# Kernel tuning notes

Measured on AMD Instinct MI355X. Metric: run time of the kernel, lower is better.

## Reference

```python
import jax, jax.numpy as jnp
import numpy as np

A = 1.0  # hard-sigmoid slope 'a'


def hard_sigm(x):
    return jnp.clip((A * x + 1.0) * 0.5, 0.0, 1.0)


def _cell(c, h_bottom, h, h_top, z, zb, U11, U21, W01, b, H):
    # batch-major equivalent of torch.mm(U, h) with h:(H,B) -> h@(U.T):(B,4H+1)
    s = (1.0 - z) * (h @ U11.T) + zb * (h_bottom @ W01.T) + b
    if U21 is not None:
        s = s + z * (h_top @ U21.T)
    f = jax.nn.sigmoid(s[:, 0:H])
    i = jax.nn.sigmoid(s[:, H:2 * H])
    o = jax.nn.sigmoid(s[:, 2 * H:3 * H])
    g = jnp.tanh(s[:, 3 * H:4 * H])
    z_hat = hard_sigm(s[:, 4 * H:4 * H + 1])  # (B,1)
    c_new = z * (i * g) + (1.0 - z) * (1.0 - zb) * c + (1.0 - z) * zb * (f * c + i * g)
    tc = jnp.tanh(c_new)
    h_new = z * o * tc + (1.0 - z) * (1.0 - zb) * h + (1.0 - z) * zb * o * tc
    return h_new, c_new, z_hat


def setup_inputs() -> dict:
    key = jax.random.key(0)
    ks = jax.random.split(key, 8)
    B, T, D = 256, 512, 128
    H1, H2 = 512, 512
    stdv = 1.0 / np.sqrt(H1)
    u = lambda k, shp: jax.random.uniform(k, shp, jnp.float32, -stdv, stdv)
    return {
        'inputs': jax.random.normal(ks[0], (B, T, D), jnp.float32),
        'U11_1': u(ks[1], (4 * H1 + 1, H1)),
        'U21_1': u(ks[2], (4 * H1 + 1, H2)),
        'W01_1': u(ks[3], (4 * H1 + 1, D)),
        'b1': u(ks[4], (4 * H1 + 1,)),
        'U11_2': u(ks[5], (4 * H2 + 1, H2)),
        'W01_2': u(ks[6], (4 * H2 + 1, H1)),
        'b2': u(ks[7], (4 * H2 + 1,)),
    }


def reference(inputs, U11_1, U21_1, W01_1, b1, U11_2, W01_2, b2):
    B, T, D = inputs.shape
    H1 = (b1.shape[0] - 1) // 4
    H2 = (b2.shape[0] - 1) // 4
    dt = inputs.dtype
    h1 = jnp.zeros((B, H1), dt); c1 = jnp.zeros((B, H1), dt); z1 = jnp.zeros((B, 1), dt)
    h2 = jnp.zeros((B, H2), dt); c2 = jnp.zeros((B, H2), dt); z2 = jnp.zeros((B, 1), dt)
    z_one = jnp.ones((B, 1), dt)

    def step(carry, x_t):
        h1, c1, z1, h2, c2, z2 = carry
        h1, c1, z1 = _cell(c1, x_t, h1, h2, z1, z_one, U11_1, U21_1, W01_1, b1, H1)
        h2, c2, z2 = _cell(c2, h1, h2, None, z2, z1, U11_2, None, W01_2, b2, H2)
        return (h1, c1, z1, h2, c2, z2), h2 * z2

    xs = jnp.swapaxes(inputs, 0, 1)  # (T,B,D)
    _, ys = jax.lax.scan(step, (h1, c1, z1, h2, c2, z2), xs)
    # dropout is identity in eval mode
    return jnp.swapaxes(ys, 0, 1)  # (B,T,H2)
```

## Files before the change

### kernel.cpp

```cpp
#include <hip/hip_runtime.h>

#define TT 512
#define BB 256
#define DD 128
#define HH 512
#define KA 1152
#define KB 1024
#define NKA 36
#define NKB 32

#define OFF_WPA  0ull
#define SZ_WPA   (128ull*NKA*2ull*512ull*2ull)
#define OFF_WPB  (OFF_WPA + SZ_WPA)
#define SZ_WPB   (128ull*NKB*2ull*512ull*2ull)
#define OFF_WZFA (OFF_WPB + SZ_WPB)
#define SZ_WZFA  (36ull*512ull*2ull)
#define OFF_WZFB (OFF_WZFA + SZ_WZFA)
#define SZ_WZFB  (32ull*512ull*2ull)
#define OFF_BP1  (OFF_WZFB + SZ_WZFB)
#define OFF_BP2  (OFF_BP1 + 8192ull)
#define OFF_BZ   (OFF_BP2 + 8192ull)
#define OFF_CNT  (OFF_BZ + 256ull)
#define OFF_A1   (OFF_CNT + 4096ull)
#define OFF_A2   (OFF_A1 + 2ull*524288ull)
#define OFF_B1   (OFF_A2 + 524288ull)
#define OFF_B2   (OFF_B1 + 2ull*524288ull)
#define OFF_END  (OFF_B2 + 524288ull)

#define PLSTR 131072

typedef __bf16 bf16x8 __attribute__((ext_vector_type(8)));
typedef float  f32x4  __attribute__((ext_vector_type(4)));
typedef unsigned short u16;

__device__ __forceinline__ u16 bf_bits(__bf16 h) {
  union { __bf16 b; u16 u; } cv; cv.b = h; return cv.u;
}
__device__ __forceinline__ float sigmoidf_(float v) { return 1.f / (1.f + __expf(-v)); }

__device__ __forceinline__ void st_uc(u16* p, u16 v) {
  unsigned vv = v;
  asm volatile("global_store_short %0, %1, off sc0 sc1" :: "v"(p), "v"(vv) : "memory");
}
__device__ __forceinline__ void split_st_uc(u16* hi, u16* lo, float v) {
  __bf16 h = (__bf16)v;
  __bf16 l = (__bf16)(v - (float)h);
  st_uc(hi, bf_bits(h));
  st_uc(lo, bf_bits(l));
}
__device__ __forceinline__ void drain_vmem() {
  asm volatile("s_waitcnt vmcnt(0)" ::: "memory");
}

__device__ __forceinline__ void gload_lds16_uc(const void* g, void* l) {
  __builtin_amdgcn_global_load_lds((const __attribute__((address_space(1))) unsigned int*)g,
                                   (__attribute__((address_space(3))) unsigned int*)l, 16, 0, 19);
}

__global__ void pack_w(const float* __restrict__ U11_1, const float* __restrict__ U21_1,
                       const float* __restrict__ W01_1, const float* __restrict__ U11_2,
                       const float* __restrict__ W01_2, u16* __restrict__ wp) {
  unsigned i = blockIdx.x * 256u + threadIdx.x;
  const unsigned NWA = 128u * NKA * 2u * 512u;
  const unsigned NWB = 128u * NKB * 2u * 512u;
  if (i >= NWA + NWB) return;
  float w; unsigned s;
  if (i < NWA) {
    unsigned lane = (i >> 3) & 63u, e = i & 7u; s = (i >> 9) & 1u;
    unsigned blk = i >> 10, kb = blk % NKA, colblk = blk / NKA;
    unsigned c = colblk * 16u + (lane & 15u);
    unsigned n = (c & 3u) * 512u + (c >> 2);
    unsigned k = kb * 32u + (lane >> 4) * 8u + e;
    w = (k < 512u)  ? U11_1[n * 512u + k]
      : (k < 1024u) ? U21_1[n * 512u + (k - 512u)]
                    : W01_1[n * 128u + (k - 1024u)];
  } else {
    unsigned j = i - NWA;
    unsigned lane = (j >> 3) & 63u, e = j & 7u; s = (j >> 9) & 1u;
    unsigned blk = j >> 10, kb = blk % NKB, colblk = blk / NKB;
    unsigned c = colblk * 16u + (lane & 15u);
    unsigned n = (c & 3u) * 512u + (c >> 2);
    unsigned k = kb * 32u + (lane >> 4) * 8u + e;
    w = (k < 512u) ? U11_2[n * 512u + k] : W01_2[n * 512u + (k - 512u)];
  }
  __bf16 hi = (__bf16)w;
  __bf16 v = s ? (__bf16)(w - (float)hi) : hi;
  wp[i] = bf_bits(v);
}

__global__ void pack_wz(const float* __restrict__ U11_1, const float* __restrict__ U21_1,
                        const float* __restrict__ W01_1, const float* __restrict__ U11_2,
                        const float* __restrict__ W01_2,
                        u16* __restrict__ wzfa, u16* __restrict__ wzfb) {
  unsigned i = blockIdx.x * 256u + threadIdx.x;
  const unsigned NZA = 36u * 512u, NZB = 32u * 512u;
  if (i >= NZA + NZB) return;
  const bool isA = i < NZA;
  unsigned j = isA ? i : i - NZA;
  unsigned e = j & 7u, lane = (j >> 3) & 63u, kb = j >> 9;
  unsigned col = lane & 15u;
  unsigned k = kb * 32u + (lane >> 4) * 8u + e;
  float wz;
  if (isA) {
    wz = (k < 512u)  ? U11_1[2048u*512u + k]
       : (k < 1024u) ? U21_1[2048u*512u + (k-512u)]
                     : W01_1[2048u*128u + (k-1024u)];
  } else {
    wz = (k < 512u) ? U11_2[2048u*512u + k] : W01_2[2048u*512u + (k-512u)];
  }
  u16 out = 0;
  if (col == 0u) out = bf_bits((__bf16)wz);
  else if (col == 1u) { __bf16 h = (__bf16)wz; out = bf_bits((__bf16)(wz - (float)h)); }
  (isA ? wzfa : wzfb)[j] = out;
}

__global__ void pack_bias(const float* __restrict__ b1, const float* __restrict__ b2,
                          float* __restrict__ bp1, float* __restrict__ bp2,
                          float* __restrict__ bz) {
  unsigned i = blockIdx.x * 256u + threadIdx.x;
  if (i < 2048u) bp1[i] = b1[(i & 3u)*512u + (i >> 2)];
  else if (i < 4096u) { unsigned c = i - 2048u; bp2[c] = b2[(c & 3u)*512u + (c >> 2)]; }
  else if (i == 4096u) bz[0] = b1[2048];
  else if (i == 4097u) bz[1] = b2[2048];
}

__global__ void init_zero(char* __restrict__ wsb) {
  size_t i = (size_t)blockIdx.x * 256u + threadIdx.x;
  size_t n = (OFF_END - OFF_CNT) / 4u;
  if (i < n) ((unsigned*)(wsb + OFF_CNT))[i] = 0u;
}

__global__ __launch_bounds__(512, 2) void hmlstm_kernel(const float* __restrict__ x,
                                                        char* __restrict__ wsb,
                                                        float* __restrict__ y) {
  const int tid  = threadIdx.x;
  const int lane = tid & 63;
  const int nw   = __builtin_amdgcn_readfirstlane(tid >> 6);
  const int bid  = blockIdx.x;
  const int ntg  = (bid & 7) * 2 + (bid >> 7);
  const int mg   = (bid >> 3) & 15;
  const int b0   = mg * 16;

  const u16* wpA  = (const u16*)(wsb + OFF_WPA);
  const u16* wpB  = (const u16*)(wsb + OFF_WPB);
  const u16* wzfA = (const u16*)(wsb + OFF_WZFA);
  const u16* wzfB = (const u16*)(wsb + OFF_WZFB);
  const float* bp1 = (const float*)(wsb + OFF_BP1);
  const float* bp2 = (const float*)(wsb + OFF_BP2);
  const float bz1 = ((const float*)(wsb + OFF_BZ))[0];
  const float bz2 = ((const float*)(wsb + OFF_BZ))[1];
  unsigned* cnt = (unsigned*)(wsb + OFF_CNT) + mg * 64;
  u16* A1b[2] = { (u16*)(wsb + OFF_A1), (u16*)(wsb + OFF_A1 + 524288ull) };
  u16* A2b    =   (u16*)(wsb + OFF_A2);
  u16* B1b[2] = { (u16*)(wsb + OFF_B1), (u16*)(wsb + OFF_B1 + 524288ull) };
  u16* B2b    =   (u16*)(wsb + OFF_B2);

  __shared__ u16 stgA[2][2][16][64][8];
  __shared__ u16 stgB[2][2][16][64][8];
  __shared__ float ls_s[16][132];
  __shared__ float zp[3][16];

  const int kgp   = lane >> 4;
  const int row16 = lane & 15;
  const int er = tid >> 5, eu = tid & 31;
  const int erow = b0 + er;
  const int ku = ntg * 32 + eu;
  const size_t pidx = ((size_t)(ku >> 3) * 256 + erow) * 8 + (ku & 7);

  const u16* wbA = wpA + (size_t)(ntg*8 + nw) * (NKA*1024u) + lane*8;
  const u16* wbB = wpB + (size_t)(ntg*8 + nw) * (NKB*1024u) + lane*8;
  const u16* wzA = wzfA + lane*8;
  const u16* wzB = wzfB + lane*8;

  float c1r = 0.f, c2r = 0.f, h2r = 0.f;
  float z1p = 0.f, z2p = 0.f, z1c = 0.f;
  unsigned bar_tgt = 16u;
  int p = 0;

  for (int t = 0; t < TT; ++t) {
    if (t == 0) {
      for (int j = 0; j < 4; ++j) {
        int i = nw*4 + j; int spl = i >> 4, kq = i & 15;
        const u16* src = A1b[0] + spl*PLSTR + ((size_t)((kq*4 + kgp)*256 + b0 + row16))*8;
        gload_lds16_uc(src, &stgA[0][spl][kq][0][0]);
      }
    }
    for (int j = 0; j < 4; ++j) {
      int i = nw*4 + j; int spl = i >> 4, kq = i & 15;
      const u16* src = A2b + spl*PLSTR + ((size_t)((kq*4 + kgp)*256 + b0 + row16))*8;
      gload_lds16_uc(src, &stgA[1][spl][kq][0][0]);
    }
    for (int j = 0; j < 4; ++j) {
      int i = nw*4 + j; int spl = i >> 4, kq = i & 15;
      const u16* src = B1b[p] + spl*PLSTR + ((size_t)((kq*4 + kgp)*256 + b0 + row16))*8;
      gload_lds16_uc(src, &stgB[0][spl][kq][0][0]);
    }
    bf16x8 xah[4], xal[4];
    {
      const float* xp = x + ((size_t)(b0 + row16) * TT + t) * DD + kgp*8;
      for (int k4 = 0; k4 < 4; ++k4) {
        float4 v0 = *(const float4*)(xp + k4*32);
        float4 v1 = *(const float4*)(xp + k4*32 + 4);
        float vv[8] = {v0.x,v0.y,v0.z,v0.w,v1.x,v1.y,v1.z,v1.w};
        for (int e = 0; e < 8; ++e) {
          __bf16 h = (__bf16)vv[e];
          xah[k4][e] = h;
          xal[k4][e] = (__bf16)(vv[e] - (float)h);
        }
      }
    }
    __syncthreads();

    {
      f32x4 acc0={0,0,0,0}, acc1={0,0,0,0}, acc2={0,0,0,0};
      f32x4 az={0,0,0,0};
      #pragma unroll 4
      for (int kb = 0; kb < 32; ++kb) {
        const u16* sa = &stgA[kb>>4][0][kb&15][lane][0];
        bf16x8 ah = *(const bf16x8*)sa;
        bf16x8 al = *(const bf16x8*)(sa + 8192);
        bf16x8 wh = *(const bf16x8*)(wbA + kb*1024);
        bf16x8 wl = *(const bf16x8*)(wbA + kb*1024 + 512);
        acc0 = __builtin_amdgcn_mfma_f32_16x16x32_bf16(ah, wh, acc0, 0, 0, 0);
        acc1 = __builtin_amdgcn_mfma_f32_16x16x32_bf16(ah, wl, acc1, 0, 0, 0);
        acc2 = __builtin_amdgcn_mfma_f32_16x16x32_bf16(al, wh, acc2, 0, 0, 0);
        if (nw == 0) { bf16x8 zf = *(const bf16x8*)(wzA + kb*512);
                       az = __builtin_amdgcn_mfma_f32_16x16x32_bf16(ah, zf, az, 0, 0, 0); }
        if (nw == 1) { bf16x8 zf = *(const bf16x8*)(wzA + kb*512);
                       az = __builtin_amdgcn_mfma_f32_16x16x32_bf16(al, zf, az, 0, 0, 0); }
      }
      for (int k4 = 0; k4 < 4; ++k4) {
        int kb = 32 + k4;
        bf16x8 ah = xah[k4], al = xal[k4];
        bf16x8 wh = *(const bf16x8*)(wbA + kb*1024);
        bf16x8 wl = *(const bf16x8*)(wbA + kb*1024 + 512);
        acc0 = __builtin_amdgcn_mfma_f32_16x16x32_bf16(ah, wh, acc0, 0, 0, 0);
        acc1 = __builtin_amdgcn_mfma_f32_16x16x32_bf16(ah, wl, acc1, 0, 0, 0);
        acc2 = __builtin_amdgcn_mfma_f32_16x16x32_bf16(al, wh, acc2, 0, 0, 0);
        if (nw == 0) { bf16x8 zf = *(const bf16x8*)(wzA + kb*512);
                       az = __builtin_amdgcn_mfma_f32_16x16x32_bf16(ah, zf, az, 0, 0, 0); }
        if (nw == 1) { bf16x8 zf = *(const bf16x8*)(wzA + kb*512);
                       az = __builtin_amdgcn_mfma_f32_16x16x32_bf16(al, zf, az, 0, 0, 0); }
      }
      f32x4 accs = acc0 + acc1; accs = accs + acc2;
      int cc = nw*16 + (lane & 15);
      int r0 = (lane >> 4) * 4;
      ls_s[r0+0][cc] = accs[0]; ls_s[r0+1][cc] = accs[1];
      ls_s[r0+2][cc] = accs[2]; ls_s[r0+3][cc] = accs[3];
      if (nw == 0 && (lane&15) == 0) {
        for (int j2 = 0; j2 < 4; ++j2) zp[0][r0+j2] = az[j2];
      }
      if (nw == 0 && (lane&15) == 1) {
        for (int j2 = 0; j2 < 4; ++j2) zp[1][r0+j2] = az[j2];
      }
      if (nw == 1 && (lane&15) == 0) {
        for (int j2 = 0; j2 < 4; ++j2) zp[2][r0+j2] = az[j2];
      }
    }
    __syncthreads();
    {
      float zs = zp[0][er] + zp[1][er] + zp[2][er] + bz1;
      float zn = fminf(fmaxf((zs + 1.f)*0.5f, 0.f), 1.f);
      float4 sv = *(const float4*)&ls_s[er][4*eu];
      float4 bb = *(const float4*)&bp1[ntg*128 + 4*eu];
      float f = sigmoidf_(sv.x + bb.x);
      float i = sigmoidf_(sv.y + bb.y);
      float o = sigmoidf_(sv.z + bb.z);
      float g = tanhf(sv.w + bb.w);
      float z = z1p;
      float ig = i * g;
      float cn = z * ig + (1.f - z) * fmaf(f, c1r, ig);
      float hn = o * tanhf(cn);
      c1r = cn;
      z1c = zn; z1p = zn;
      u16* a1w = A1b[p ^ 1];
      split_st_uc(a1w + pidx, a1w + PLSTR + pidx, (1.f - zn) * hn);
      split_st_uc(B2b + pidx, B2b + PLSTR + pidx, zn * hn);
    }
    drain_vmem();
    __syncthreads();
    if (tid == 0) {
      __hip_atomic_fetch_add(cnt, 1u, __ATOMIC_RELAXED, __HIP_MEMORY_SCOPE_AGENT);
      while (__hip_atomic_load(cnt, __ATOMIC_RELAXED, __HIP_MEMORY_SCOPE_AGENT) < bar_tgt)
        __builtin_amdgcn_s_sleep(1);
    }
    bar_tgt += 16u;
    __builtin_amdgcn_s_barrier();

    for (int j = 0; j < 4; ++j) {
      int i = nw*4 + j; int spl = i >> 4, kq = i & 15;
      const u16* src = B2b + spl*PLSTR + ((size_t)((kq*4 + kgp)*256 + b0 + row16))*8;
      gload_lds16_uc(src, &stgB[1][spl][kq][0][0]);
    }
    for (int j = 0; j < 4; ++j) {
      int i = nw*4 + j; int spl = i >> 4, kq = i & 15;
      const u16* src = A1b[p ^ 1] + spl*PLSTR + ((size_t)((kq*4 + kgp)*256 + b0 + row16))*8;
      gload_lds16_uc(src, &stgA[0][spl][kq][0][0]);
    }
    __syncthreads();

    {
      f32x4 acc0={0,0,0,0}, acc1={0,0,0,0}, acc2={0,0,0,0};
      f32x4 az={0,0,0,0};
      #pragma unroll 4
      for (int kb = 0; kb < 32; ++kb) {
        const u16* sa = &stgB[kb>>4][0][kb&15][lane][0];
        bf16x8 ah = *(const bf16x8*)sa;
        bf16x8 al = *(const bf16x8*)(sa + 8192);
        bf16x8 wh = *(const bf16x8*)(wbB + kb*1024);
        bf16x8 wl = *(const bf16x8*)(wbB + kb*1024 + 512);
        acc0 = __builtin_amdgcn_mfma_f32_16x16x32_bf16(ah, wh, acc0, 0, 0, 0);
        acc1 = __builtin_amdgcn_mfma_f32_16x16x32_bf16(ah, wl, acc1, 0, 0, 0);
        acc2 = __builtin_amdgcn_mfma_f32_16x16x32_bf16(al, wh, acc2, 0, 0, 0);
        if (nw == 0) { bf16x8 zf = *(const bf16x8*)(wzB + kb*512);
                       az = __builtin_amdgcn_mfma_f32_16x16x32_bf16(ah, zf, az, 0, 0, 0); }
        if (nw == 1) { bf16x8 zf = *(const bf16x8*)(wzB + kb*512);
                       az = __builtin_amdgcn_mfma_f32_16x16x32_bf16(al, zf, az, 0, 0, 0); }
      }
      f32x4 accs = acc0 + acc1; accs = accs + acc2;
      int cc = nw*16 + (lane & 15);
      int r0 = (lane >> 4) * 4;
      ls_s[r0+0][cc] = accs[0]; ls_s[r0+1][cc] = accs[1];
      ls_s[r0+2][cc] = accs[2]; ls_s[r0+3][cc] = accs[3];
      if (nw == 0 && (lane&15) == 0) {
        for (int j2 = 0; j2 < 4; ++j2) zp[0][r0+j2] = az[j2];
      }
      if (nw == 0 && (lane&15) == 1) {
        for (int j2 = 0; j2 < 4; ++j2) zp[1][r0+j2] = az[j2];
      }
      if (nw == 1 && (lane&15) == 0) {
        for (int j2 = 0; j2 < 4; ++j2) zp[2][r0+j2] = az[j2];
      }
    }
    __syncthreads();
    {
      float zs = zp[0][er] + zp[1][er] + zp[2][er] + bz2;
      float z2n_ = fminf(fmaxf((zs + 1.f)*0.5f, 0.f), 1.f);
      float4 sv = *(const float4*)&ls_s[er][4*eu];
      float4 bb = *(const float4*)&bp2[ntg*128 + 4*eu];
      float f = sigmoidf_(sv.x + bb.x);
      float i = sigmoidf_(sv.y + bb.y);
      float o = sigmoidf_(sv.z + bb.z);
      float g = tanhf(sv.w + bb.w);
      float z = z2p, zb = z1c;
      float ig = i * g;
      float cn = z*ig + (1.f-z)*(1.f-zb)*c2r + (1.f-z)*zb*fmaf(f, c2r, ig);
      float tc = tanhf(cn);
      float ot = o * tc;
      float hn = z*ot + (1.f-z)*(1.f-zb)*h2r + (1.f-z)*zb*ot;
      c2r = cn; h2r = hn;
      z2p = z2n_;
      y[((size_t)erow * TT + t) * HH + ku] = hn * z2n_;
      u16* b1w = B1b[p ^ 1];
      split_st_uc(b1w + pidx, b1w + PLSTR + pidx, (1.f - z2n_) * hn);
      split_st_uc(A2b + pidx, A2b + PLSTR + pidx, z1c * hn);
    }
    drain_vmem();
    __syncthreads();
    if (tid == 0) {
      __hip_atomic_fetch_add(cnt, 1u, __ATOMIC_RELAXED, __HIP_MEMORY_SCOPE_AGENT);
      while (__hip_atomic_load(cnt, __ATOMIC_RELAXED, __HIP_MEMORY_SCOPE_AGENT) < bar_tgt)
        __builtin_amdgcn_s_sleep(1);
    }
    bar_tgt += 16u;
    __builtin_amdgcn_s_barrier();

    p ^= 1;
  }
}

extern "C" void kernel_launch(void* const* d_in, const int* in_sizes, int n_in,
                              void* d_out, int out_size, void* d_ws, size_t ws_size,
                              hipStream_t stream) {
  const float* x     = (const float*)d_in[0];
  const float* U11_1 = (const float*)d_in[1];
  const float* U21_1 = (const float*)d_in[2];
  const float* W01_1 = (const float*)d_in[3];
  const float* b1    = (const float*)d_in[4];
  const float* U11_2 = (const float*)d_in[5];
  const float* W01_2 = (const float*)d_in[6];
  const float* b2    = (const float*)d_in[7];
  char*  wsb = (char*)d_ws;
  float* y   = (float*)d_out;
  (void)in_sizes; (void)n_in; (void)out_size; (void)ws_size;

  u16* wp    = (u16*)(wsb + OFF_WPA);
  u16* wzfa  = (u16*)(wsb + OFF_WZFA);
  u16* wzfb  = (u16*)(wsb + OFF_WZFB);
  float* bp1 = (float*)(wsb + OFF_BP1);
  float* bp2 = (float*)(wsb + OFF_BP2);
  float* bz  = (float*)(wsb + OFF_BZ);

  const unsigned NW = 128u*NKA*2u*512u + 128u*NKB*2u*512u;
  hipLaunchKernelGGL(pack_w, dim3((NW + 255u)/256u), dim3(256), 0, stream,
                     U11_1, U21_1, W01_1, U11_2, W01_2, wp);
  const unsigned NZ = 36u*512u + 32u*512u;
  hipLaunchKernelGGL(pack_wz, dim3((NZ + 255u)/256u), dim3(256), 0, stream,
                     U11_1, U21_1, W01_1, U11_2, W01_2, wzfa, wzfb);
  hipLaunchKernelGGL(pack_bias, dim3(17), dim3(256), 0, stream, b1, b2, bp1, bp2, bz);
  const unsigned n_zero_words = (unsigned)((OFF_END - OFF_CNT) / 4u);
  hipLaunchKernelGGL(init_zero, dim3((n_zero_words + 255u)/256u), dim3(256), 0, stream, wsb);

  const float* xq = x;
  char* wsq = wsb;
  float* yq = y;
  void* kargs[] = { (void*)&xq, (void*)&wsq, (void*)&yq };
  hipLaunchCooperativeKernel((void*)hmlstm_kernel, dim3(256), dim3(512), kargs, 0, stream);
}
```

Before: 15.56 ms.

## Replace atomic-counter grid barrier with per-block flag array and wave-wide polling

The atomic fetch-add counter barrier across the 16 blocks of a batch group is replaced by a flag array: each block writes its phase number to its own slot, and wave 0 polls all 16 slots with uncached loads and a ballot. This removes contention on one atomic and lets a single poll observe every peer. The global-to-LDS load cache-policy bits change from 19 to 17, and the MFMA inner loops unroll 8 instead of 4. The flag protocol depends on uncached stores becoming visible in order after the data stores, and the larger unroll raises register pressure.

```diff
diff --git a/kernel.cpp b/kernel.cpp
--- a/kernel.cpp
+++ b/kernel.cpp
@@ -42,6 +42,15 @@
   unsigned vv = v;
   asm volatile("global_store_short %0, %1, off sc0 sc1" :: "v"(p), "v"(vv) : "memory");
 }
+__device__ __forceinline__ void st_uc_u32(unsigned* p, unsigned v) {
+  asm volatile("global_store_dword %0, %1, off sc0 sc1" :: "v"(p), "v"(v) : "memory");
+}
+__device__ __forceinline__ unsigned ld_uc_u32(const unsigned* p) {
+  unsigned v;
+  asm volatile("global_load_dword %0, %1, off sc0 sc1\n\ts_waitcnt vmcnt(0)"
+               : "=v"(v) : "v"(p) : "memory");
+  return v;
+}
 __device__ __forceinline__ void split_st_uc(u16* hi, u16* lo, float v) {
   __bf16 h = (__bf16)v;
   __bf16 l = (__bf16)(v - (float)h);
@@ -54,7 +63,7 @@
 
 __device__ __forceinline__ void gload_lds16_uc(const void* g, void* l) {
   __builtin_amdgcn_global_load_lds((const __attribute__((address_space(1))) unsigned int*)g,
-                                   (__attribute__((address_space(3))) unsigned int*)l, 16, 0, 19);
+                                   (__attribute__((address_space(3))) unsigned int*)l, 16, 0, 17);
 }
 
 __global__ void pack_w(const float* __restrict__ U11_1, const float* __restrict__ U21_1,
@@ -149,7 +158,7 @@
   const float* bp2 = (const float*)(wsb + OFF_BP2);
   const float bz1 = ((const float*)(wsb + OFF_BZ))[0];
   const float bz2 = ((const float*)(wsb + OFF_BZ))[1];
-  unsigned* cnt = (unsigned*)(wsb + OFF_CNT) + mg * 64;
+  unsigned* flags = (unsigned*)(wsb + OFF_CNT) + mg * 64;
   u16* A1b[2] = { (u16*)(wsb + OFF_A1), (u16*)(wsb + OFF_A1 + 524288ull) };
   u16* A2b    =   (u16*)(wsb + OFF_A2);
   u16* B1b[2] = { (u16*)(wsb + OFF_B1), (u16*)(wsb + OFF_B1 + 524288ull) };
@@ -174,7 +183,6 @@
 
   float c1r = 0.f, c2r = 0.f, h2r = 0.f;
   float z1p = 0.f, z2p = 0.f, z1c = 0.f;
-  unsigned bar_tgt = 16u;
   int p = 0;
 
   for (int t = 0; t < TT; ++t) {
@@ -214,7 +222,7 @@
     {
       f32x4 acc0={0,0,0,0}, acc1={0,0,0,0}, acc2={0,0,0,0};
       f32x4 az={0,0,0,0};
-      #pragma unroll 4
+      #pragma unroll 8
       for (int kb = 0; kb < 32; ++kb) {
         const u16* sa = &stgA[kb>>4][0][kb&15][lane][0];
         bf16x8 ah = *(const bf16x8*)sa;
@@ -279,13 +287,20 @@
     }
     drain_vmem();
     __syncthreads();
-    if (tid == 0) {
-      __hip_atomic_fetch_add(cnt, 1u, __ATOMIC_RELAXED, __HIP_MEMORY_SCOPE_AGENT);
-      while (__hip_atomic_load(cnt, __ATOMIC_RELAXED, __HIP_MEMORY_SCOPE_AGENT) < bar_tgt)
-        __builtin_amdgcn_s_sleep(1);
-    }
-    bar_tgt += 16u;
-    __builtin_amdgcn_s_barrier();
+    {
+      const unsigned tgt = 2u*(unsigned)t + 1u;
+      if (nw == 0) {
+        if (lane == 0) st_uc_u32(&flags[ntg], tgt);
+        const unsigned* fp = flags + (lane & 15);
+        const bool mine = lane < 16;
+        while (true) {
+          unsigned v = mine ? ld_uc_u32(fp) : tgt;
+          if (__ballot(v >= tgt) == ~0ull) break;
+          __builtin_amdgcn_s_sleep(1);
+        }
+      }
+      __builtin_amdgcn_s_barrier();
+    }
 
     for (int j = 0; j < 4; ++j) {
       int i = nw*4 + j; int spl = i >> 4, kq = i & 15;
@@ -302,7 +317,7 @@
     {
       f32x4 acc0={0,0,0,0}, acc1={0,0,0,0}, acc2={0,0,0,0};
       f32x4 az={0,0,0,0};
-      #pragma unroll 4
+      #pragma unroll 8
       for (int kb = 0; kb < 32; ++kb) {
         const u16* sa = &stgB[kb>>4][0][kb&15][lane][0];
         bf16x8 ah = *(const bf16x8*)sa;
@@ -357,13 +372,20 @@
     }
     drain_vmem();
     __syncthreads();
-    if (tid == 0) {
-      __hip_atomic_fetch_add(cnt, 1u, __ATOMIC_RELAXED, __HIP_MEMORY_SCOPE_AGENT);
-      while (__hip_atomic_load(cnt, __ATOMIC_RELAXED, __HIP_MEMORY_SCOPE_AGENT) < bar_tgt)
-        __builtin_amdgcn_s_sleep(1);
-    }
-    bar_tgt += 16u;
-    __builtin_amdgcn_s_barrier();
+    {
+      const unsigned tgt = 2u*(unsigned)t + 2u;
+      if (nw == 0) {
+        if (lane == 0) st_uc_u32(&flags[ntg], tgt);
+        const unsigned* fp = flags + (lane & 15);
+        const bool mine = lane < 16;
+        while (true) {
+          unsigned v = mine ? ld_uc_u32(fp) : tgt;
+          if (__ballot(v >= tgt) == ~0ull) break;
+          __builtin_amdgcn_s_sleep(1);
+        }
+      }
+      __builtin_amdgcn_s_barrier();
+    }
 
     p ^= 1;
   }
```

After: 22.44 ms. 44.2% more time.

## Retile persistent HM-LSTM blocks to 32 batch rows by 16 hidden units

Applied to the files above, without the earlier changes.

Changes the per-block tile from 16 batch rows × 32 hidden units to 32 rows × 16 units, arranging the 8 waves as a 2×4 grid over M and N. Each block now loads a full 32-row activation slab into one unified staging buffer per layer phase, and the previously prefetched A1 load for the next step is folded into the per-phase load. The intent is to halve the weight fragments each block streams per step and to share activation loads across M, at the cost of more activation staging per block and 32 blocks per batch group joining each grid barrier.

```diff
diff --git a/kernel.cpp b/kernel.cpp
--- a/kernel.cpp
+++ b/kernel.cpp
@@ -136,10 +136,14 @@
   const int tid  = threadIdx.x;
   const int lane = tid & 63;
   const int nw   = __builtin_amdgcn_readfirstlane(tid >> 6);
+  const int mf   = nw >> 2;
+  const int nf   = nw & 3;
   const int bid  = blockIdx.x;
-  const int ntg  = (bid & 7) * 2 + (bid >> 7);
-  const int mg   = (bid >> 3) & 15;
-  const int b0   = mg * 16;
+  const int xcd  = bid & 7;
+  const int q    = (bid >> 3) & 3;
+  const int mg   = bid >> 5;
+  const int ntg  = xcd * 4 + q;
+  const int b0   = mg * 32;
 
   const u16* wpA  = (const u16*)(wsb + OFF_WPA);
   const u16* wpB  = (const u16*)(wsb + OFF_WPB);
@@ -155,49 +159,48 @@
   u16* B1b[2] = { (u16*)(wsb + OFF_B1), (u16*)(wsb + OFF_B1 + 524288ull) };
   u16* B2b    =   (u16*)(wsb + OFF_B2);
 
-  __shared__ u16 stgA[2][2][16][64][8];
-  __shared__ u16 stgB[2][2][16][64][8];
-  __shared__ float ls_s[16][132];
-  __shared__ float zp[3][16];
+  __shared__ u16 stg[32][2][2][64][8];
+  __shared__ float ls_s[32][68];
+  __shared__ float zp[3][32];
 
   const int kgp   = lane >> 4;
   const int row16 = lane & 15;
-  const int er = tid >> 5, eu = tid & 31;
+  const int er = tid >> 4, eu = tid & 15;
   const int erow = b0 + er;
-  const int ku = ntg * 32 + eu;
+  const int ku = ntg * 16 + eu;
   const size_t pidx = ((size_t)(ku >> 3) * 256 + erow) * 8 + (ku & 7);
 
-  const u16* wbA = wpA + (size_t)(ntg*8 + nw) * (NKA*1024u) + lane*8;
-  const u16* wbB = wpB + (size_t)(ntg*8 + nw) * (NKB*1024u) + lane*8;
+  const u16* wbA = wpA + (size_t)(ntg*4 + nf) * (NKA*1024u) + lane*8;
+  const u16* wbB = wpB + (size_t)(ntg*4 + nf) * (NKB*1024u) + lane*8;
   const u16* wzA = wzfA + lane*8;
   const u16* wzB = wzfB + lane*8;
 
   float c1r = 0.f, c2r = 0.f, h2r = 0.f;
   float z1p = 0.f, z2p = 0.f, z1c = 0.f;
-  unsigned bar_tgt = 16u;
+  unsigned bar_tgt = 32u;
   int p = 0;
 
+  const int xrow = b0 + mf*16 + row16;
+
   for (int t = 0; t < TT; ++t) {
-    if (t == 0) {
-      for (int j = 0; j < 4; ++j) {
-        int i = nw*4 + j; int spl = i >> 4, kq = i & 15;
-        const u16* src = A1b[0] + spl*PLSTR + ((size_t)((kq*4 + kgp)*256 + b0 + row16))*8;
-        gload_lds16_uc(src, &stgA[0][spl][kq][0][0]);
-      }
-    }
-    for (int j = 0; j < 4; ++j) {
-      int i = nw*4 + j; int spl = i >> 4, kq = i & 15;
-      const u16* src = A2b + spl*PLSTR + ((size_t)((kq*4 + kgp)*256 + b0 + row16))*8;
-      gload_lds16_uc(src, &stgA[1][spl][kq][0][0]);
-    }
-    for (int j = 0; j < 4; ++j) {
-      int i = nw*4 + j; int spl = i >> 4, kq = i & 15;
-      const u16* src = B1b[p] + spl*PLSTR + ((size_t)((kq*4 + kgp)*256 + b0 + row16))*8;
-      gload_lds16_uc(src, &stgB[0][spl][kq][0][0]);
+    {
+      const u16* first  = A1b[p];
+      const u16* second = A2b;
+      for (int j = 0; j < 16; ++j) {
+        int idx = nw*16 + j;
+        int kb  = idx >> 2;
+        int spl = (idx >> 1) & 1;
+        int mfh = idx & 1;
+        const u16* base = (kb < 16) ? first : second;
+        int kq = kb & 15;
+        const u16* src = base + spl*PLSTR
+                       + ((size_t)((kq*4 + kgp)*256 + b0 + mfh*16 + row16))*8;
+        gload_lds16_uc(src, &stg[kb][spl][mfh][0][0]);
+      }
     }
     bf16x8 xah[4], xal[4];
     {
-      const float* xp = x + ((size_t)(b0 + row16) * TT + t) * DD + kgp*8;
+      const float* xp = x + ((size_t)xrow * TT + t) * DD + kgp*8;
       for (int k4 = 0; k4 < 4; ++k4) {
         float4 v0 = *(const float4*)(xp + k4*32);
         float4 v1 = *(const float4*)(xp + k4*32 + 4);
@@ -216,17 +219,17 @@
       f32x4 az={0,0,0,0};
       #pragma unroll 4
       for (int kb = 0; kb < 32; ++kb) {
-        const u16* sa = &stgA[kb>>4][0][kb&15][lane][0];
+        const u16* sa = &stg[kb][0][mf][lane][0];
         bf16x8 ah = *(const bf16x8*)sa;
-        bf16x8 al = *(const bf16x8*)(sa + 8192);
+        bf16x8 al = *(const bf16x8*)(sa + 1024);
         bf16x8 wh = *(const bf16x8*)(wbA + kb*1024);
         bf16x8 wl = *(const bf16x8*)(wbA + kb*1024 + 512);
         acc0 = __builtin_amdgcn_mfma_f32_16x16x32_bf16(ah, wh, acc0, 0, 0, 0);
         acc1 = __builtin_amdgcn_mfma_f32_16x16x32_bf16(ah, wl, acc1, 0, 0, 0);
         acc2 = __builtin_amdgcn_mfma_f32_16x16x32_bf16(al, wh, acc2, 0, 0, 0);
-        if (nw == 0) { bf16x8 zf = *(const bf16x8*)(wzA + kb*512);
+        if (nf == 0) { bf16x8 zf = *(const bf16x8*)(wzA + kb*512);
                        az = __builtin_amdgcn_mfma_f32_16x16x32_bf16(ah, zf, az, 0, 0, 0); }
-        if (nw == 1) { bf16x8 zf = *(const bf16x8*)(wzA + kb*512);
+        if (nf == 1) { bf16x8 zf = *(const bf16x8*)(wzA + kb*512);
                        az = __builtin_amdgcn_mfma_f32_16x16x32_bf16(al, zf, az, 0, 0, 0); }
       }
       for (int k4 = 0; k4 < 4; ++k4) {
@@ -237,23 +240,23 @@
         acc0 = __builtin_amdgcn_mfma_f32_16x16x32_bf16(ah, wh, acc0, 0, 0, 0);
         acc1 = __builtin_amdgcn_mfma_f32_16x16x32_bf16(ah, wl, acc1, 0, 0, 0);
         acc2 = __builtin_amdgcn_mfma_f32_16x16x32_bf16(al, wh, acc2, 0, 0, 0);
-        if (nw == 0) { bf16x8 zf = *(const bf16x8*)(wzA + kb*512);
+        if (nf == 0) { bf16x8 zf = *(const bf16x8*)(wzA + kb*512);
                        az = __builtin_amdgcn_mfma_f32_16x16x32_bf16(ah, zf, az, 0, 0, 0); }
-        if (nw == 1) { bf16x8 zf = *(const bf16x8*)(wzA + kb*512);
+        if (nf == 1) { bf16x8 zf = *(const bf16x8*)(wzA + kb*512);
                        az = __builtin_amdgcn_mfma_f32_16x16x32_bf16(al, zf, az, 0, 0, 0); }
       }
       f32x4 accs = acc0 + acc1; accs = accs + acc2;
-      int cc = nw*16 + (lane & 15);
-      int r0 = (lane >> 4) * 4;
+      int cc = nf*16 + (lane & 15);
+      int r0 = mf*16 + (lane >> 4) * 4;
       ls_s[r0+0][cc] = accs[0]; ls_s[r0+1][cc] = accs[1];
       ls_s[r0+2][cc] = accs[2]; ls_s[r0+3][cc] = accs[3];
-      if (nw == 0 && (lane&15) == 0) {
+      if (nf == 0 && (lane&15) == 0) {
         for (int j2 = 0; j2 < 4; ++j2) zp[0][r0+j2] = az[j2];
       }
-      if (nw == 0 && (lane&15) == 1) {
+      if (nf == 0 && (lane&15) == 1) {
         for (int j2 = 0; j2 < 4; ++j2) zp[1][r0+j2] = az[j2];
       }
-      if (nw == 1 && (lane&15) == 0) {
+      if (nf == 1 && (lane&15) == 0) {
         for (int j2 = 0; j2 < 4; ++j2) zp[2][r0+j2] = az[j2];
       }
     }
@@ -262,7 +265,7 @@
       float zs = zp[0][er] + zp[1][er] + zp[2][er] + bz1;
       float zn = fminf(fmaxf((zs + 1.f)*0.5f, 0.f), 1.f);
       float4 sv = *(const float4*)&ls_s[er][4*eu];
-      float4 bb = *(const float4*)&bp1[ntg*128 + 4*eu];
+      float4 bb = *(const float4*)&bp1[ntg*64 + 4*eu];
       float f = sigmoidf_(sv.x + bb.x);
       float i = sigmoidf_(sv.y + bb.y);
       float o = sigmoidf_(sv.z + bb.z);
@@ -284,18 +287,23 @@
       while (__hip_atomic_load(cnt, __ATOMIC_RELAXED, __HIP_MEMORY_SCOPE_AGENT) < bar_tgt)
         __builtin_amdgcn_s_sleep(1);
     }
-    bar_tgt += 16u;
+    bar_tgt += 32u;
     __builtin_amdgcn_s_barrier();
 
-    for (int j = 0; j < 4; ++j) {
-      int i = nw*4 + j; int spl = i >> 4, kq = i & 15;
-      const u16* src = B2b + spl*PLSTR + ((size_t)((kq*4 + kgp)*256 + b0 + row16))*8;
-      gload_lds16_uc(src, &stgB[1][spl][kq][0][0]);
-    }
-    for (int j = 0; j < 4; ++j) {
-      int i = nw*4 + j; int spl = i >> 4, kq = i & 15;
-      const u16* src = A1b[p ^ 1] + spl*PLSTR + ((size_t)((kq*4 + kgp)*256 + b0 + row16))*8;
-      gload_lds16_uc(src, &stgA[0][spl][kq][0][0]);
+    {
+      const u16* first  = B1b[p];
+      const u16* second = B2b;
+      for (int j = 0; j < 16; ++j) {
+        int idx = nw*16 + j;
+        int kb  = idx >> 2;
+        int spl = (idx >> 1) & 1;
+        int mfh = idx & 1;
+        const u16* base = (kb < 16) ? first : second;
+        int kq = kb & 15;
+        const u16* src = base + spl*PLSTR
+                       + ((size_t)((kq*4 + kgp)*256 + b0 + mfh*16 + row16))*8;
+        gload_lds16_uc(src, &stg[kb][spl][mfh][0][0]);
+      }
     }
     __syncthreads();
 
@@ -304,31 +312,31 @@
       f32x4 az={0,0,0,0};
       #pragma unroll 4
       for (int kb = 0; kb < 32; ++kb) {
-        const u16* sa = &stgB[kb>>4][0][kb&15][lane][0];
+        const u16* sa = &stg[kb][0][mf][lane][0];
         bf16x8 ah = *(const bf16x8*)sa;
-        bf16x8 al = *(const bf16x8*)(sa + 8192);
+        bf16x8 al = *(const bf16x8*)(sa + 1024);
         bf16x8 wh = *(const bf16x8*)(wbB + kb*1024);
         bf16x8 wl = *(const bf16x8*)(wbB + kb*1024 + 512);
         acc0 = __builtin_amdgcn_mfma_f32_16x16x32_bf16(ah, wh, acc0, 0, 0, 0);
         acc1 = __builtin_amdgcn_mfma_f32_16x16x32_bf16(ah, wl, acc1, 0, 0, 0);
         acc2 = __builtin_amdgcn_mfma_f32_16x16x32_bf16(al, wh, acc2, 0, 0, 0);
-        if (nw == 0) { bf16x8 zf = *(const bf16x8*)(wzB + kb*512);
+        if (nf == 0) { bf16x8 zf = *(const bf16x8*)(wzB + kb*512);
                        az = __builtin_amdgcn_mfma_f32_16x16x32_bf16(ah, zf, az, 0, 0, 0); }
-        if (nw == 1) { bf16x8 zf = *(const bf16x8*)(wzB + kb*512);
+        if (nf == 1) { bf16x8 zf = *(const bf16x8*)(wzB + kb*512);
                        az = __builtin_amdgcn_mfma_f32_16x16x32_bf16(al, zf, az, 0, 0, 0); }
       }
       f32x4 accs = acc0 + acc1; accs = accs + acc2;
-      int cc = nw*16 + (lane & 15);
-      int r0 = (lane >> 4) * 4;
+      int cc = nf*16 + (lane & 15);
+      int r0 = mf*16 + (lane >> 4) * 4;
       ls_s[r0+0][cc] = accs[0]; ls_s[r0+1][cc] = accs[1];
       ls_s[r0+2][cc] = accs[2]; ls_s[r0+3][cc] = accs[3];
-      if (nw == 0 && (lane&15) == 0) {
+      if (nf == 0 && (lane&15) == 0) {
         for (int j2 = 0; j2 < 4; ++j2) zp[0][r0+j2] = az[j2];
       }
-      if (nw == 0 && (lane&15) == 1) {
+      if (nf == 0 && (lane&15) == 1) {
         for (int j2 = 0; j2 < 4; ++j2) zp[1][r0+j2] = az[j2];
       }
-      if (nw == 1 && (lane&15) == 0) {
+      if (nf == 1 && (lane&15) == 0) {
         for (int j2 = 0; j2 < 4; ++j2) zp[2][r0+j2] = az[j2];
       }
     }
@@ -337,7 +345,7 @@
       float zs = zp[0][er] + zp[1][er] + zp[2][er] + bz2;
       float z2n_ = fminf(fmaxf((zs + 1.f)*0.5f, 0.f), 1.f);
       float4 sv = *(const float4*)&ls_s[er][4*eu];
-      float4 bb = *(const float4*)&bp2[ntg*128 + 4*eu];
+      float4 bb = *(const float4*)&bp2[ntg*64 + 4*eu];
       float f = sigmoidf_(sv.x + bb.x);
       float i = sigmoidf_(sv.y + bb.y);
       float o = sigmoidf_(sv.z + bb.z);
@@ -362,7 +370,7 @@
       while (__hip_atomic_load(cnt, __ATOMIC_RELAXED, __HIP_MEMORY_SCOPE_AGENT) < bar_tgt)
         __builtin_amdgcn_s_sleep(1);
     }
-    bar_tgt += 16u;
+    bar_tgt += 32u;
     __builtin_amdgcn_s_barrier();
 
     p ^= 1;
```

Measured after the change: 18.38 ms. 18.1% more time.

## Split work over 512 blocks of 4 waves with chunked double-buffered LDS staging

Applied to the files above, without the earlier changes.

The recurrent kernel is repartitioned from 256 blocks of 8 waves to 512 blocks of 4 waves. Each block now covers 16 hidden units instead of 32, and the grid barrier counts 32 arrivals per group. The activation staging now streams K in four double-buffered chunks through a smaller LDS buffer, so loads overlap the MFMAs instead of loading everything up front. The launch also changes from cooperative to a plain launch, which risks a deadlock in the spin barrier if not all 512 blocks are resident at once, and adds more synchronisation points per step.

```diff
diff --git a/kernel.cpp b/kernel.cpp
--- a/kernel.cpp
+++ b/kernel.cpp
@@ -55,6 +55,20 @@
 __device__ __forceinline__ void gload_lds16_uc(const void* g, void* l) {
   __builtin_amdgcn_global_load_lds((const __attribute__((address_space(1))) unsigned int*)g,
                                    (__attribute__((address_space(3))) unsigned int*)l, 16, 0, 19);
+}
+
+__device__ __forceinline__ void stage_chunk(const u16* first, const u16* second, int c,
+                                            int nw, int kgp, int grow, u16* buf) {
+  for (int j = 0; j < 4; ++j) {
+    int idx = nw*4 + j;
+    int spl = idx >> 3;
+    int kbl = idx & 7;
+    int kb  = c*8 + kbl;
+    const u16* base = (kb < 16) ? first : second;
+    int kq = kb & 15;
+    const u16* src = base + spl*PLSTR + ((size_t)((kq*4 + kgp)*256 + grow))*8;
+    gload_lds16_uc(src, buf + ((size_t)(spl*8 + kbl)*64)*8);
+  }
 }
 
 __global__ void pack_w(const float* __restrict__ U11_1, const float* __restrict__ U21_1,
@@ -130,15 +144,17 @@
   if (i < n) ((unsigned*)(wsb + OFF_CNT))[i] = 0u;
 }
 
-__global__ __launch_bounds__(512, 2) void hmlstm_kernel(const float* __restrict__ x,
+__global__ __launch_bounds__(256, 2) void hmlstm_kernel(const float* __restrict__ x,
                                                         char* __restrict__ wsb,
                                                         float* __restrict__ y) {
   const int tid  = threadIdx.x;
   const int lane = tid & 63;
   const int nw   = __builtin_amdgcn_readfirstlane(tid >> 6);
   const int bid  = blockIdx.x;
-  const int ntg  = (bid & 7) * 2 + (bid >> 7);
-  const int mg   = (bid >> 3) & 15;
+  const int xcd  = bid & 7;
+  const int q    = (bid >> 3) & 3;
+  const int mg   = bid >> 5;
+  const int ntg  = xcd * 4 + q;
   const int b0   = mg * 16;
 
   const u16* wpA  = (const u16*)(wsb + OFF_WPA);
@@ -155,79 +171,73 @@
   u16* B1b[2] = { (u16*)(wsb + OFF_B1), (u16*)(wsb + OFF_B1 + 524288ull) };
   u16* B2b    =   (u16*)(wsb + OFF_B2);
 
-  __shared__ u16 stgA[2][2][16][64][8];
-  __shared__ u16 stgB[2][2][16][64][8];
-  __shared__ float ls_s[16][132];
+  __shared__ u16 stg[2][2][8][64][8];
+  __shared__ float ls_s[16][68];
   __shared__ float zp[3][16];
 
   const int kgp   = lane >> 4;
   const int row16 = lane & 15;
-  const int er = tid >> 5, eu = tid & 31;
+  const int er = tid >> 4, eu = tid & 15;
   const int erow = b0 + er;
-  const int ku = ntg * 32 + eu;
+  const int ku = ntg * 16 + eu;
   const size_t pidx = ((size_t)(ku >> 3) * 256 + erow) * 8 + (ku & 7);
 
-  const u16* wbA = wpA + (size_t)(ntg*8 + nw) * (NKA*1024u) + lane*8;
-  const u16* wbB = wpB + (size_t)(ntg*8 + nw) * (NKB*1024u) + lane*8;
+  const u16* wbA = wpA + (size_t)(ntg*4 + nw) * (NKA*1024u) + lane*8;
+  const u16* wbB = wpB + (size_t)(ntg*4 + nw) * (NKB*1024u) + lane*8;
   const u16* wzA = wzfA + lane*8;
   const u16* wzB = wzfB + lane*8;
 
   float c1r = 0.f, c2r = 0.f, h2r = 0.f;
   float z1p = 0.f, z2p = 0.f, z1c = 0.f;
-  unsigned bar_tgt = 16u;
+  unsigned bar_tgt = 32u;
   int p = 0;
 
+  const int grow = b0 + row16;
+
   for (int t = 0; t < TT; ++t) {
-    if (t == 0) {
-      for (int j = 0; j < 4; ++j) {
-        int i = nw*4 + j; int spl = i >> 4, kq = i & 15;
-        const u16* src = A1b[0] + spl*PLSTR + ((size_t)((kq*4 + kgp)*256 + b0 + row16))*8;
-        gload_lds16_uc(src, &stgA[0][spl][kq][0][0]);
-      }
-    }
-    for (int j = 0; j < 4; ++j) {
-      int i = nw*4 + j; int spl = i >> 4, kq = i & 15;
-      const u16* src = A2b + spl*PLSTR + ((size_t)((kq*4 + kgp)*256 + b0 + row16))*8;
-      gload_lds16_uc(src, &stgA[1][spl][kq][0][0]);
-    }
-    for (int j = 0; j < 4; ++j) {
-      int i = nw*4 + j; int spl = i >> 4, kq = i & 15;
-      const u16* src = B1b[p] + spl*PLSTR + ((size_t)((kq*4 + kgp)*256 + b0 + row16))*8;
-      gload_lds16_uc(src, &stgB[0][spl][kq][0][0]);
-    }
-    bf16x8 xah[4], xal[4];
     {
-      const float* xp = x + ((size_t)(b0 + row16) * TT + t) * DD + kgp*8;
-      for (int k4 = 0; k4 < 4; ++k4) {
-        float4 v0 = *(const float4*)(xp + k4*32);
-        float4 v1 = *(const float4*)(xp + k4*32 + 4);
-        float vv[8] = {v0.x,v0.y,v0.z,v0.w,v1.x,v1.y,v1.z,v1.w};
-        for (int e = 0; e < 8; ++e) {
-          __bf16 h = (__bf16)vv[e];
-          xah[k4][e] = h;
-          xal[k4][e] = (__bf16)(vv[e] - (float)h);
-        }
-      }
-    }
-    __syncthreads();
-
-    {
+      const u16* first  = A1b[p];
+      const u16* second = A2b;
       f32x4 acc0={0,0,0,0}, acc1={0,0,0,0}, acc2={0,0,0,0};
       f32x4 az={0,0,0,0};
-      #pragma unroll 4
-      for (int kb = 0; kb < 32; ++kb) {
-        const u16* sa = &stgA[kb>>4][0][kb&15][lane][0];
-        bf16x8 ah = *(const bf16x8*)sa;
-        bf16x8 al = *(const bf16x8*)(sa + 8192);
-        bf16x8 wh = *(const bf16x8*)(wbA + kb*1024);
-        bf16x8 wl = *(const bf16x8*)(wbA + kb*1024 + 512);
-        acc0 = __builtin_amdgcn_mfma_f32_16x16x32_bf16(ah, wh, acc0, 0, 0, 0);
-        acc1 = __builtin_amdgcn_mfma_f32_16x16x32_bf16(ah, wl, acc1, 0, 0, 0);
-        acc2 = __builtin_amdgcn_mfma_f32_16x16x32_bf16(al, wh, acc2, 0, 0, 0);
-        if (nw == 0) { bf16x8 zf = *(const bf16x8*)(wzA + kb*512);
-                       az = __builtin_amdgcn_mfma_f32_16x16x32_bf16(ah, zf, az, 0, 0, 0); }
-        if (nw == 1) { bf16x8 zf = *(const bf16x8*)(wzA + kb*512);
-                       az = __builtin_amdgcn_mfma_f32_16x16x32_bf16(al, zf, az, 0, 0, 0); }
+
+      stage_chunk(first, second, 0, nw, kgp, grow, &stg[0][0][0][0][0]);
+      bf16x8 xah[4], xal[4];
+      {
+        const float* xp = x + ((size_t)grow * TT + t) * DD + kgp*8;
+        for (int k4 = 0; k4 < 4; ++k4) {
+          float4 v0 = *(const float4*)(xp + k4*32);
+          float4 v1 = *(const float4*)(xp + k4*32 + 4);
+          float vv[8] = {v0.x,v0.y,v0.z,v0.w,v1.x,v1.y,v1.z,v1.w};
+          for (int e = 0; e < 8; ++e) {
+            __bf16 h = (__bf16)vv[e];
+            xah[k4][e] = h;
+            xal[k4][e] = (__bf16)(vv[e] - (float)h);
+          }
+        }
+      }
+      __syncthreads();
+
+      for (int c = 0; c < 4; ++c) {
+        const u16* cur = &stg[c & 1][0][0][0][0];
+        if (c < 3) stage_chunk(first, second, c + 1, nw, kgp, grow, &stg[(c + 1) & 1][0][0][0][0]);
+        #pragma unroll
+        for (int kbl = 0; kbl < 8; ++kbl) {
+          int kb = c*8 + kbl;
+          const u16* sa = cur + ((size_t)kbl*64 + lane)*8;
+          bf16x8 ah = *(const bf16x8*)sa;
+          bf16x8 al = *(const bf16x8*)(sa + 4096);
+          bf16x8 wh = *(const bf16x8*)(wbA + kb*1024);
+          bf16x8 wl = *(const bf16x8*)(wbA + kb*1024 + 512);
+          acc0 = __builtin_amdgcn_mfma_f32_16x16x32_bf16(ah, wh, acc0, 0, 0, 0);
+          acc1 = __builtin_amdgcn_mfma_f32_16x16x32_bf16(ah, wl, acc1, 0, 0, 0);
+          acc2 = __builtin_amdgcn_mfma_f32_16x16x32_bf16(al, wh, acc2, 0, 0, 0);
+          if (nw == 0) { bf16x8 zf = *(const bf16x8*)(wzA + kb*512);
+                         az = __builtin_amdgcn_mfma_f32_16x16x32_bf16(ah, zf, az, 0, 0, 0); }
+          if (nw == 1) { bf16x8 zf = *(const bf16x8*)(wzA + kb*512);
+                         az = __builtin_amdgcn_mfma_f32_16x16x32_bf16(al, zf, az, 0, 0, 0); }
+        }
+        __syncthreads();
       }
       for (int k4 = 0; k4 < 4; ++k4) {
         int kb = 32 + k4;
@@ -262,7 +272,7 @@
       float zs = zp[0][er] + zp[1][er] + zp[2][er] + bz1;
       float zn = fminf(fmaxf((zs + 1.f)*0.5f, 0.f), 1.f);
       float4 sv = *(const float4*)&ls_s[er][4*eu];
-      float4 bb = *(const float4*)&bp1[ntg*128 + 4*eu];
+      float4 bb = *(const float4*)&bp1[ntg*64 + 4*eu];
       float f = sigmoidf_(sv.x + bb.x);
       float i = sigmoidf_(sv.y + bb.y);
       float o = sigmoidf_(sv.z + bb.z);
@@ -284,38 +294,38 @@
       while (__hip_atomic_load(cnt, __ATOMIC_RELAXED, __HIP_MEMORY_SCOPE_AGENT) < bar_tgt)
         __builtin_amdgcn_s_sleep(1);
     }
-    bar_tgt += 16u;
+    bar_tgt += 32u;
     __builtin_amdgcn_s_barrier();
 
-    for (int j = 0; j < 4; ++j) {
-      int i = nw*4 + j; int spl = i >> 4, kq = i & 15;
-      const u16* src = B2b + spl*PLSTR + ((size_t)((kq*4 + kgp)*256 + b0 + row16))*8;
-      gload_lds16_uc(src, &stgB[1][spl][kq][0][0]);
-    }
-    for (int j = 0; j < 4; ++j) {
-      int i = nw*4 + j; int spl = i >> 4, kq = i & 15;
-      const u16* src = A1b[p ^ 1] + spl*PLSTR + ((size_t)((kq*4 + kgp)*256 + b0 + row16))*8;
-      gload_lds16_uc(src, &stgA[0][spl][kq][0][0]);
-    }
-    __syncthreads();
-
     {
+      const u16* first  = B1b[p];
+      const u16* second = B2b;
       f32x4 acc0={0,0,0,0}, acc1={0,0,0,0}, acc2={0,0,0,0};
       f32x4 az={0,0,0,0};
-      #pragma unroll 4
-      for (int kb = 0; kb < 32; ++kb) {
-        const u16* sa = &stgB[kb>>4][0][kb&15][lane][0];
-        bf16x8 ah = *(const bf16x8*)sa;
-        bf16x8 al = *(const bf16x8*)(sa + 8192);
-        bf16x8 wh = *(const bf16x8*)(wbB + kb*1024);
-        bf16x8 wl = *(const bf16x8*)(wbB + kb*1024 + 512);
-        acc0 = __builtin_amdgcn_mfma_f32_16x16x32_bf16(ah, wh, acc0, 0, 0, 0);
-        acc1 = __builtin_amdgcn_mfma_f32_16x16x32_bf16(ah, wl, acc1, 0, 0, 0);
-        acc2 = __builtin_amdgcn_mfma_f32_16x16x32_bf16(al, wh, acc2, 0, 0, 0);
-        if (nw == 0) { bf16x8 zf = *(const bf16x8*)(wzB + kb*512);
-                       az = __builtin_amdgcn_mfma_f32_16x16x32_bf16(ah, zf, az, 0, 0, 0); }
-        if (nw == 1) { bf16x8 zf = *(const bf16x8*)(wzB + kb*512);
-                       az = __builtin_amdgcn_mfma_f32_16x16x32_bf16(al, zf, az, 0, 0, 0); }
+
+      stage_chunk(first, second, 0, nw, kgp, grow, &stg[0][0][0][0][0]);
+      __syncthreads();
+
+      for (int c = 0; c < 4; ++c) {
+        const u16* cur = &stg[c & 1][0][0][0][0];
+        if (c < 3) stage_chunk(first, second, c + 1, nw, kgp, grow, &stg[(c + 1) & 1][0][0][0][0]);
+        #pragma unroll
+        for (int kbl = 0; kbl < 8; ++kbl) {
+          int kb = c*8 + kbl;
+          const u16* sa = cur + ((size_t)kbl*64 + lane)*8;
+          bf16x8 ah = *(const bf16x8*)sa;
+          bf16x8 al = *(const bf16x8*)(sa + 4096);
+          bf16x8 wh = *(const bf16x8*)(wbB + kb*1024);
+          bf16x8 wl = *(const bf16x8*)(wbB + kb*1024 + 512);
+          acc0 = __builtin_amdgcn_mfma_f32_16x16x32_bf16(ah, wh, acc0, 0, 0, 0);
+          acc1 = __builtin_amdgcn_mfma_f32_16x16x32_bf16(ah, wl, acc1, 0, 0, 0);
+          acc2 = __builtin_amdgcn_mfma_f32_16x16x32_bf16(al, wh, acc2, 0, 0, 0);
+          if (nw == 0) { bf16x8 zf = *(const bf16x8*)(wzB + kb*512);
+                         az = __builtin_amdgcn_mfma_f32_16x16x32_bf16(ah, zf, az, 0, 0, 0); }
+          if (nw == 1) { bf16x8 zf = *(const bf16x8*)(wzB + kb*512);
+                         az = __builtin_amdgcn_mfma_f32_16x16x32_bf16(al, zf, az, 0, 0, 0); }
+        }
+        __syncthreads();
       }
       f32x4 accs = acc0 + acc1; accs = accs + acc2;
       int cc = nw*16 + (lane & 15);
@@ -337,7 +347,7 @@
       float zs = zp[0][er] + zp[1][er] + zp[2][er] + bz2;
       float z2n_ = fminf(fmaxf((zs + 1.f)*0.5f, 0.f), 1.f);
       float4 sv = *(const float4*)&ls_s[er][4*eu];
-      float4 bb = *(const float4*)&bp2[ntg*128 + 4*eu];
+      float4 bb = *(const float4*)&bp2[ntg*64 + 4*eu];
       float f = sigmoidf_(sv.x + bb.x);
       float i = sigmoidf_(sv.y + bb.y);
       float o = sigmoidf_(sv.z + bb.z);
@@ -362,7 +372,7 @@
       while (__hip_atomic_load(cnt, __ATOMIC_RELAXED, __HIP_MEMORY_SCOPE_AGENT) < bar_tgt)
         __builtin_amdgcn_s_sleep(1);
     }
-    bar_tgt += 16u;
+    bar_tgt += 32u;
     __builtin_amdgcn_s_barrier();
 
     p ^= 1;
@@ -401,9 +411,5 @@
   const unsigned n_zero_words = (unsigned)((OFF_END - OFF_CNT) / 4u);
   hipLaunchKernelGGL(init_zero, dim3((n_zero_words + 255u)/256u), dim3(256), 0, stream, wsb);
 
-  const float* xq = x;
-  char* wsq = wsb;
-  float* yq = y;
-  void* kargs[] = { (void*)&xq, (void*)&wsq, (void*)&yq };
-  hipLaunchCooperativeKernel((void*)hmlstm_kernel, dim3(256), dim3(512), kargs, 0, stream);
-}
+  hipLaunchKernelGGL(hmlstm_kernel, dim3(512), dim3(256), 0, stream, x, wsb, y);
+}
```

New measurement: 47.58 ms. 206% more time.
